# Performance work log

Hardware: AMD Instinct MI355X
Metric: run time of the kernel (lower is better)

## Reference

```python
import jax, jax.numpy as jnp
import numpy as np
import math

SIGMA_DATA = 0.5
SIGMA_MIN = 0.002
SIGMA_MAX = 80.0
B = 32768
STATE = 256
ACT = 64
TD = 16
E = 16
H = 256  # moe hidden = gate_dim = output_dim = hidden_dim//4
IN = STATE + ACT + TD  # 336
TOP_K = 4


def mish(x):
    return x * jnp.tanh(jax.nn.softplus(x))


def setup_inputs() -> dict:
    key = jax.random.key(0)
    ks = jax.random.split(key, 20)
    def xavier(k, shape):
        fan_in, fan_out = shape[-2], shape[-1]
        lim = math.sqrt(6.0 / (fan_in + fan_out))
        return jax.random.uniform(k, shape, jnp.float32, -lim, lim)
    inp = {
        "x": jax.random.normal(ks[0], (B, ACT), jnp.float32),
        "sigma": jax.random.uniform(ks[1], (B,), jnp.float32) * (SIGMA_MAX - SIGMA_MIN) + SIGMA_MIN,
        "state": jax.random.normal(ks[2], (B, STATE), jnp.float32),
        # time MLP: Linear(16,32), Mish, Linear(32,16)
        "tW1": xavier(ks[3], (TD, 2 * TD)), "tb1": jnp.zeros((2 * TD,), jnp.float32),
        "tW2": xavier(ks[4], (2 * TD, TD)), "tb2": jnp.zeros((TD,), jnp.float32),
        # gate: Linear(IN, H), ReLU, (dropout eval), Linear(H, E)
        "gW1": xavier(ks[5], (IN, H)), "gb1": jnp.zeros((H,), jnp.float32),
        "gW2": xavier(ks[6], (H, E)), "gb2": jnp.zeros((E,), jnp.float32),
        # 16 stacked expert MLPs: IN->H->H->H with Mish after each Linear
        "eW1": xavier(ks[7], (E, IN, H)), "eb1": jnp.zeros((E, H), jnp.float32),
        "eW2": xavier(ks[8], (E, H, H)), "eb2": jnp.zeros((E, H), jnp.float32),
        "eW3": xavier(ks[9], (E, H, H)), "eb3": jnp.zeros((E, H), jnp.float32),
        # final layer: Linear(H, ACT)
        "fW": xavier(ks[10], (H, ACT)), "fb": jnp.zeros((ACT,), jnp.float32),
    }
    return inp


def reference(x, sigma, state, tW1, tb1, tW2, tb2, gW1, gb1, gW2, gb2,
              eW1, eb1, eW2, eb2, eW3, eb3, fW, fb):
    # --- consistency-model scalings (boundary condition) ---
    c_skip = SIGMA_DATA ** 2 / ((sigma - SIGMA_MIN) ** 2 + SIGMA_DATA ** 2)
    c_out = (sigma - SIGMA_MIN) * SIGMA_DATA * jax.lax.rsqrt(sigma ** 2 + SIGMA_DATA ** 2)
    c_in = jax.lax.rsqrt(sigma ** 2 + SIGMA_DATA ** 2)
    rescaled_t = 1000.0 * 0.25 * jnp.log(sigma + 1e-44)

    x_in = c_in[:, None] * x

    # --- sinusoidal time embedding (dim=16) + time MLP ---
    half = TD // 2
    freqs = jnp.exp(jnp.arange(half, dtype=jnp.float32) * (-math.log(10000.0) / (half - 1)))
    ang = rescaled_t[:, None] * freqs[None, :]           # [B, 8]
    pe = jnp.concatenate([jnp.sin(ang), jnp.cos(ang)], axis=-1)  # [B, 16]
    t = mish(pe @ tW1 + tb1) @ tW2 + tb2                 # [B, 16]

    inp = jnp.concatenate([x_in, t, state], axis=1)      # [B, 336]

    # --- gate (eval mode: dropout off) ---
    g = jax.nn.relu(inp @ gW1 + gb1) @ gW2 + gb2         # [B, E]
    gate_scores = jax.nn.softmax(g, axis=1)
    top_k_scores, top_k_idx = jax.lax.top_k(gate_scores, TOP_K)  # [B, K]

    # --- run ALL experts densely (as the original does) ---
    h = mish(jnp.einsum('bi,eih->beh', inp, eW1) + eb1)  # [B, E, H]
    h = mish(jnp.einsum('beh,ehk->bek', h, eW2) + eb2)
    expert_out = mish(jnp.einsum('beh,eho->beo', h, eW3) + eb3)  # [B, E, H]

    # --- gather top-k, scale by normalized gate scores, combine ---
    sel = jnp.take_along_axis(expert_out, top_k_idx[:, :, None], axis=1)  # [B, K, H]
    scaled = sel * top_k_scores[:, :, None]
    scaled = scaled / (jnp.sum(top_k_scores, axis=1, keepdims=True)[:, :, None] + 1e-9)
    combined = jnp.sum(scaled, axis=1)                   # [B, H]

    # --- auxiliary loss ---
    one_hot = jax.nn.one_hot(top_k_idx, E, dtype=jnp.float32)  # [B, K, E]
    expert_load = jnp.sum(one_hot, axis=(0, 1)) / (x.shape[0] + 1e-9)
    load_balancing_loss = jnp.var(expert_load, ddof=1)   # torch .var() is unbiased
    entropy = -jnp.mean(jnp.sum(gate_scores * jnp.log(gate_scores + 1e-9), axis=1))
    aux_loss = load_balancing_loss + entropy

    model_out = combined @ fW + fb                       # [B, ACT]
    denoised = c_out[:, None] * model_out + c_skip[:, None] * x
    denoised = jnp.clip(denoised, -1.0, 1.0)             # clip_denoised=True
    return denoised, aux_loss
```

## Files before the change

kernel.cpp:

```cpp
#include <hip/hip_runtime.h>
#include <math.h>

#define BN 32768
#define INDP 352
#define HD 256
#define AD 64
#define EN 16
#define TM 64
#define STOT (BN * 4)

typedef __attribute__((ext_vector_type(8))) short s8v;
typedef __attribute__((ext_vector_type(4))) float f4v;
typedef unsigned short u16;

__device__ __forceinline__ u16 f2bf(float x) {
  unsigned u = __float_as_uint(x);
  return (u16)((u + 0x7fffu + ((u >> 16) & 1u)) >> 16);
}
__device__ __forceinline__ float bf2f(u16 h) { return __uint_as_float(((unsigned)h) << 16); }
__device__ __forceinline__ float rcpf(float a) { float r; asm("v_rcp_f32 %0, %1" : "=v"(r) : "v"(a)); return r; }
__device__ __forceinline__ float mishf(float x) {
  float xc = fminf(x, 30.f);
  float u = __expf(xc);
  float w = fmaf(u, u, u + u);
  return x * w * rcpf(w + 2.f);
}
__device__ __forceinline__ f4v mfma16(s8v a, s8v b, f4v c) {
  return __builtin_amdgcn_mfma_f32_16x16x32_bf16(a, b, c, 0, 0, 0);
}
__device__ __forceinline__ void pack8(const u16* q, u16* d) {
  uint4 u;
  u.x = q[0] | ((unsigned)q[1] << 16); u.y = q[2] | ((unsigned)q[3] << 16);
  u.z = q[4] | ((unsigned)q[5] << 16); u.w = q[6] | ((unsigned)q[7] << 16);
  *(uint4*)d = u;
}

__global__ void k_init(float* __restrict__ out, int* __restrict__ counts,
                       int* __restrict__ cursor, float* __restrict__ ent) {
  int i = blockIdx.x * 256 + threadIdx.x;
  if (i < BN * AD) out[i] = 0.f;
  if (i < 16) { counts[i] = 0; cursor[i] = 0; }
  if (i == 16) *ent = 0.f;
}

__global__ void k_prep(const float* __restrict__ src, u16* __restrict__ dst,
                       int Ksrc, int Spad, int NT, int N,
                       long sStride, long dStride, int NP, int total) {
  int idx = blockIdx.x * 256 + threadIdx.x;
  if (idx >= total) return;
  int l = idx & 63;
  int t = idx >> 6;
  int nt = t % NT; t /= NT;
  int s = t % Spad; t /= Spad;
  int m = t;
  const float* sp = src + (size_t)m * sStride;
  int n = nt * 16 + (l & 15);
  int kb = s * 32 + (l >> 4) * 8;
  u16 q0[8], q1[8], q2[8];
  #pragma unroll
  for (int i = 0; i < 8; ++i) {
    int k = kb + i;
    float v = (k < Ksrc) ? sp[(size_t)k * N + n] : 0.f;
    u16 a = f2bf(v); float r1 = v - bf2f(a);
    u16 b = f2bf(r1); float r2 = r1 - bf2f(b);
    q0[i] = a; q1[i] = b; q2[i] = f2bf(r2);
  }
  u16* d = dst + (size_t)m * dStride + (size_t)((s * NT + nt) * NP) * 512 + l * 8;
  pack8(q0, d);
  pack8(q1, d + 512);
  if (NP == 3) pack8(q2, d + 1024);
}

__global__ void k_time_inp(const float* __restrict__ x, const float* __restrict__ sigma,
                           const float* __restrict__ state,
                           const float* __restrict__ tW1, const float* __restrict__ tb1,
                           const float* __restrict__ tW2, const float* __restrict__ tb2,
                           u16* __restrict__ p0, u16* __restrict__ p1, u16* __restrict__ p2) {
  const int wv = threadIdx.x >> 6;
  const int lane = threadIdx.x & 63;
  const int row = blockIdx.x * 4 + wv;
  const float sg = sigma[row];
  const float rt = 250.0f * logf(sg + 1e-44f);
  float pe = 0.f;
  if (lane < 16) {
    int j = lane & 7;
    float f = expf(-1.3157629102823121f * (float)j);
    float ang = rt * f;
    pe = (lane < 8) ? sinf(ang) : cosf(ang);
  }
  float h1;
  {
    float acc = 0.f;
    int j = lane & 31;
    #pragma unroll
    for (int i = 0; i < 16; ++i) {
      float p = __shfl(pe, i, 64);
      acc = fmaf(p, tW1[i * 32 + j], acc);
    }
    acc += tb1[j];
    float sp = log1pf(expf(acc));
    h1 = acc * tanhf(sp);
  }
  float t2;
  {
    float acc = 0.f;
    int j = lane & 15;
    #pragma unroll
    for (int i = 0; i < 32; ++i) {
      float h = __shfl(h1, i, 64);
      acc = fmaf(h, tW2[i * 16 + j], acc);
    }
    t2 = acc + tb2[j];
  }
  const float c_in = rsqrtf(sg * sg + 0.25f);
  u16* r0 = p0 + (size_t)row * INDP;
  u16* r1 = p1 + (size_t)row * INDP;
  u16* r2 = p2 + (size_t)row * INDP;
  auto wsplit = [&](int c, float v) {
    u16 a = f2bf(v); float ra = v - bf2f(a);
    u16 b = f2bf(ra); float rb = ra - bf2f(b);
    r0[c] = a; r1[c] = b; r2[c] = f2bf(rb);
  };
  wsplit(lane, c_in * x[row * 64 + lane]);
  if (lane < 16) wsplit(64 + lane, t2);
  #pragma unroll
  for (int r = 0; r < 4; ++r)
    wsplit(80 + r * 64 + lane, state[(size_t)row * 256 + r * 64 + lane]);
  if (lane < 16) { r0[336 + lane] = 0; r1[336 + lane] = 0; r2[336 + lane] = 0; }
}

__global__ __launch_bounds__(256) void k_gate(
    const u16* __restrict__ p0, const u16* __restrict__ p1, const u16* __restrict__ p2,
    const u16* __restrict__ gW1b, const float* __restrict__ gb1,
    const float* __restrict__ gW2, const float* __restrict__ gb2,
    int* __restrict__ topk_idx, float* __restrict__ topk_w,
    int* __restrict__ counts, float* __restrict__ ent_sum) {
  __shared__ float sH[TM * 257];
  __shared__ float sB2[256 * 16];
  __shared__ float sLog[TM * 16];
  __shared__ int scnt[16];
  const int tid = threadIdx.x;
  const int l = tid & 63, w = tid >> 6;
  const int g = l >> 4, r16 = l & 15;
  const int row0 = blockIdx.x * TM;
  if (tid < 16) scnt[tid] = 0;

  f4v acc[4][4];
  #pragma unroll
  for (int i = 0; i < 4; ++i)
    #pragma unroll
    for (int j = 0; j < 4; ++j) acc[i][j] = (f4v){0.f, 0.f, 0.f, 0.f};

  for (int s = 0; s < 11; ++s) {
    s8v a0[4], a1[4], a2[4], b0[4], b1[4], b2[4];
    #pragma unroll
    for (int mt = 0; mt < 4; ++mt) {
      size_t off = (size_t)(row0 + mt * 16 + r16) * INDP + s * 32 + g * 8;
      a0[mt] = *(const s8v*)(p0 + off);
      a1[mt] = *(const s8v*)(p1 + off);
      a2[mt] = *(const s8v*)(p2 + off);
    }
    #pragma unroll
    for (int j = 0; j < 4; ++j) {
      const u16* pb = gW1b + (size_t)((s * 16 + w * 4 + j) * 3) * 512 + l * 8;
      b0[j] = *(const s8v*)pb;
      b1[j] = *(const s8v*)(pb + 512);
      b2[j] = *(const s8v*)(pb + 1024);
    }
    #pragma unroll
    for (int mt = 0; mt < 4; ++mt)
      #pragma unroll
      for (int j = 0; j < 4; ++j) {
        acc[mt][j] = mfma16(a0[mt], b0[j], acc[mt][j]);
        acc[mt][j] = mfma16(a0[mt], b1[j], acc[mt][j]);
        acc[mt][j] = mfma16(a1[mt], b0[j], acc[mt][j]);
        acc[mt][j] = mfma16(a1[mt], b1[j], acc[mt][j]);
        acc[mt][j] = mfma16(a0[mt], b2[j], acc[mt][j]);
        acc[mt][j] = mfma16(a2[mt], b0[j], acc[mt][j]);
      }
  }
  float bj[4];
  #pragma unroll
  for (int j = 0; j < 4; ++j) bj[j] = gb1[w * 64 + j * 16 + r16];
  #pragma unroll
  for (int mt = 0; mt < 4; ++mt)
    #pragma unroll
    for (int j = 0; j < 4; ++j)
      #pragma unroll
      for (int r = 0; r < 4; ++r) {
        int row = mt * 16 + g * 4 + r;
        sH[row * 257 + w * 64 + j * 16 + r16] = fmaxf(acc[mt][j][r] + bj[j], 0.f);
      }
  #pragma unroll
  for (int it = 0; it < 4; ++it) {
    int idx = tid + it * 256;
    *(float4*)&sB2[idx * 4] = *(const float4*)(gW2 + (size_t)idx * 4);
  }
  __syncthreads();
  {
    const int rr = tid >> 2, q = tid & 3;
    float g0 = 0.f, g1 = 0.f, g2 = 0.f, g3 = 0.f;
    for (int k = 0; k < 256; ++k) {
      float a = sH[rr * 257 + k];
      float4 bv = *(const float4*)&sB2[k * 16 + q * 4];
      g0 = fmaf(a, bv.x, g0); g1 = fmaf(a, bv.y, g1);
      g2 = fmaf(a, bv.z, g2); g3 = fmaf(a, bv.w, g3);
    }
    sLog[rr * 16 + q * 4 + 0] = g0 + gb2[q * 4 + 0];
    sLog[rr * 16 + q * 4 + 1] = g1 + gb2[q * 4 + 1];
    sLog[rr * 16 + q * 4 + 2] = g2 + gb2[q * 4 + 2];
    sLog[rr * 16 + q * 4 + 3] = g3 + gb2[q * 4 + 3];
  }
  __syncthreads();
  float entc = 0.f;
  if (tid < 64) {
    const int row = row0 + tid;
    float gx[16], mx = -1e30f;
    #pragma unroll
    for (int e = 0; e < 16; ++e) { gx[e] = sLog[tid * 16 + e]; mx = fmaxf(mx, gx[e]); }
    float p[16], s = 0.f;
    #pragma unroll
    for (int e = 0; e < 16; ++e) { p[e] = expf(gx[e] - mx); s += p[e]; }
    const float inv = 1.f / s;
    #pragma unroll
    for (int e = 0; e < 16; ++e) {
      float pr = p[e] * inv;
      entc -= pr * logf(pr + 1e-9f);
    }
    int idxs[4]; float scs[4];
    unsigned used = 0;
    float wsum = 1e-9f;
    #pragma unroll
    for (int k = 0; k < 4; ++k) {
      int be = 0; float bv = -1.f;
      #pragma unroll
      for (int e = 0; e < 16; ++e) {
        float pr = p[e] * inv;
        if (!((used >> e) & 1u) && pr > bv) { bv = pr; be = e; }
      }
      used |= (1u << be);
      idxs[k] = be; scs[k] = bv;
      wsum += bv;
    }
    #pragma unroll
    for (int k = 0; k < 4; ++k) {
      topk_idx[row * 4 + k] = idxs[k];
      topk_w[row * 4 + k] = scs[k] / wsum;
      atomicAdd(&scnt[idxs[k]], 1);
    }
    #pragma unroll
    for (int off = 32; off > 0; off >>= 1) entc += __shfl_down(entc, off, 64);
  }
  __syncthreads();
  if (tid == 0) atomicAdd(ent_sum, entc);
  if (tid < 16 && scnt[tid] > 0) atomicAdd(&counts[tid], scnt[tid]);
}

__global__ void k_aux(const int* __restrict__ counts, const float* __restrict__ ent_sum,
                      int* __restrict__ offsets, int* __restrict__ tbk,
                      float* __restrict__ aux_out) {
  if (threadIdx.x == 0) {
    int off = 0, t = 0;
    float load[16], mean = 0.f;
    for (int e = 0; e < 16; ++e) {
      offsets[e] = off; tbk[e] = t;
      int c = counts[e];
      off += c;
      t += (c + TM - 1) / TM;
      load[e] = (float)c / (32768.0f + 1e-9f);
      mean += load[e];
    }
    offsets[16] = off; tbk[16] = t;
    mean *= (1.f / 16.f);
    float var = 0.f;
    for (int e = 0; e < 16; ++e) { float d = load[e] - mean; var += d * d; }
    var *= (1.f / 15.f);
    *aux_out = var + ent_sum[0] * (1.0f / 32768.0f);
  }
}

__global__ void k_scatter(const int* __restrict__ topk_idx, const float* __restrict__ topk_w,
                          const int* __restrict__ offsets, int* __restrict__ cursor,
                          int* __restrict__ slot_row, float* __restrict__ slot_w) {
  __shared__ int cnt[16];
  __shared__ int base[16];
  const int tid = threadIdx.x;
  if (tid < 16) cnt[tid] = 0;
  __syncthreads();
  const int row = blockIdx.x * 256 + tid;
  int e4[4]; float w4[4]; int lp[4];
  #pragma unroll
  for (int k = 0; k < 4; ++k) {
    e4[k] = topk_idx[row * 4 + k];
    w4[k] = topk_w[row * 4 + k];
    lp[k] = atomicAdd(&cnt[e4[k]], 1);
  }
  __syncthreads();
  if (tid < 16) base[tid] = atomicAdd(&cursor[tid], cnt[tid]);
  __syncthreads();
  #pragma unroll
  for (int k = 0; k < 4; ++k) {
    int s = offsets[e4[k]] + base[e4[k]] + lp[k];
    slot_row[s] = row;
    slot_w[s] = w4[k];
  }
}

__global__ __launch_bounds__(256, 2) void k_expert(
    const u16* __restrict__ inpHi, const u16* __restrict__ inpLo,
    const u16* __restrict__ eW1b, const float* __restrict__ eb1,
    const u16* __restrict__ eW2b, const float* __restrict__ eb2,
    const u16* __restrict__ eW3b, const float* __restrict__ eb3,
    const u16* __restrict__ fWb,
    const int* __restrict__ offsets, const int* __restrict__ counts,
    const int* __restrict__ tbk, const int* __restrict__ slot_row,
    const float* __restrict__ slot_w, float* __restrict__ out) {
  __shared__ __align__(16) u16 sHi[TM * 256];
  __shared__ __align__(16) u16 sLo[TM * 256];
  __shared__ int sRows[TM];
  __shared__ float sWv[TM];

  const int bid = blockIdx.x;
  if (bid >= tbk[16]) return;
  int e = 0;
  #pragma unroll
  for (int i = 1; i < 16; ++i)
    if (bid >= tbk[i]) e = i;
  const int tile = bid - tbk[e];
  const int cnt = counts[e];
  const int s0 = offsets[e] + tile * TM;
  const int nr = min(TM, cnt - tile * TM);
  const int tid = threadIdx.x;
  const int l = tid & 63, w = tid >> 6;
  const int g = l >> 4, r16 = l & 15;
  const int swz = (r16 & 7) << 3;

  if (tid < TM) {
    sRows[tid] = (tid < nr) ? slot_row[s0 + tid] : slot_row[s0];
    sWv[tid] = (tid < nr) ? slot_w[s0 + tid] : 0.f;
  }
  __syncthreads();

  size_t rbase[4];
  #pragma unroll
  for (int mt = 0; mt < 4; ++mt) rbase[mt] = (size_t)sRows[mt * 16 + r16] * INDP;

  f4v acc[4][4];
  #pragma unroll
  for (int i = 0; i < 4; ++i)
    #pragma unroll
    for (int j = 0; j < 4; ++j) acc[i][j] = (f4v){0.f, 0.f, 0.f, 0.f};

  const u16* W1 = eW1b + (size_t)e * 180224;
  for (int s = 0; s < 11; ++s) {
    s8v ah[4], al[4], bh[4], bl[4];
    #pragma unroll
    for (int mt = 0; mt < 4; ++mt) {
      size_t off = rbase[mt] + s * 32 + g * 8;
      ah[mt] = *(const s8v*)(inpHi + off);
      al[mt] = *(const s8v*)(inpLo + off);
    }
    #pragma unroll
    for (int j = 0; j < 4; ++j) {
      const u16* pb = W1 + (size_t)((s * 16 + w * 4 + j) * 2) * 512 + l * 8;
      bh[j] = *(const s8v*)pb;
      bl[j] = *(const s8v*)(pb + 512);
    }
    #pragma unroll
    for (int mt = 0; mt < 4; ++mt)
      #pragma unroll
      for (int j = 0; j < 4; ++j) {
        acc[mt][j] = mfma16(ah[mt], bh[j], acc[mt][j]);
        acc[mt][j] = mfma16(al[mt], bh[j], acc[mt][j]);
        acc[mt][j] = mfma16(ah[mt], bl[j], acc[mt][j]);
      }
  }
  {
    const float* b1 = eb1 + e * HD;
    float bj[4];
    #pragma unroll
    for (int j = 0; j < 4; ++j) bj[j] = b1[w * 64 + j * 16 + r16];
    #pragma unroll
    for (int mt = 0; mt < 4; ++mt)
      #pragma unroll
      for (int j = 0; j < 4; ++j)
        #pragma unroll
        for (int r = 0; r < 4; ++r) {
          int row = mt * 16 + g * 4 + r;
          int col = w * 64 + j * 16 + r16;
          float v = mishf(acc[mt][j][r] + bj[j]);
          u16 h = f2bf(v);
          int ec = col ^ ((row & 7) << 3);
          sHi[row * 256 + ec] = h;
          sLo[row * 256 + ec] = f2bf(v - bf2f(h));
        }
  }
  __syncthreads();

  #pragma unroll 1
  for (int L = 0; L < 2; ++L) {
    const u16* Wb = (L == 0 ? eW2b : eW3b) + (size_t)e * 131072;
    const float* bb = (L == 0 ? eb2 : eb3) + e * HD;
    f4v a2[4][4];
    #pragma unroll
    for (int i = 0; i < 4; ++i)
      #pragma unroll
      for (int j = 0; j < 4; ++j) a2[i][j] = (f4v){0.f, 0.f, 0.f, 0.f};
    #pragma unroll 2
    for (int s = 0; s < 8; ++s) {
      s8v ah[4], al[4], bh[4], bl[4];
      #pragma unroll
      for (int mt = 0; mt < 4; ++mt) {
        int row = mt * 16 + r16;
        int ec = (s * 32 + g * 8) ^ swz;
        ah[mt] = *(const s8v*)&sHi[row * 256 + ec];
        al[mt] = *(const s8v*)&sLo[row * 256 + ec];
      }
      #pragma unroll
      for (int j = 0; j < 4; ++j) {
        const u16* pb = Wb + (size_t)((s * 16 + w * 4 + j) * 2) * 512 + l * 8;
        bh[j] = *(const s8v*)pb;
        bl[j] = *(const s8v*)(pb + 512);
      }
      #pragma unroll
      for (int mt = 0; mt < 4; ++mt)
        #pragma unroll
        for (int j = 0; j < 4; ++j) {
          a2[mt][j] = mfma16(ah[mt], bh[j], a2[mt][j]);
          a2[mt][j] = mfma16(al[mt], bh[j], a2[mt][j]);
          a2[mt][j] = mfma16(ah[mt], bl[j], a2[mt][j]);
        }
    }
    __syncthreads();
    float bj[4];
    #pragma unroll
    for (int j = 0; j < 4; ++j) bj[j] = bb[w * 64 + j * 16 + r16];
    #pragma unroll
    for (int mt = 0; mt < 4; ++mt)
      #pragma unroll
      for (int j = 0; j < 4; ++j)
        #pragma unroll
        for (int r = 0; r < 4; ++r) {
          int row = mt * 16 + g * 4 + r;
          int col = w * 64 + j * 16 + r16;
          float v = mishf(a2[mt][j][r] + bj[j]);
          u16 h = f2bf(v);
          int ec = col ^ ((row & 7) << 3);
          sHi[row * 256 + ec] = h;
          sLo[row * 256 + ec] = f2bf(v - bf2f(h));
        }
    __syncthreads();
  }

  f4v a3[4];
  #pragma unroll
  for (int i = 0; i < 4; ++i) a3[i] = (f4v){0.f, 0.f, 0.f, 0.f};
  #pragma unroll 2
  for (int s = 0; s < 8; ++s) {
    s8v ah[4], al[4];
    #pragma unroll
    for (int mt = 0; mt < 4; ++mt) {
      int row = mt * 16 + r16;
      int ec = (s * 32 + g * 8) ^ swz;
      ah[mt] = *(const s8v*)&sHi[row * 256 + ec];
      al[mt] = *(const s8v*)&sLo[row * 256 + ec];
    }
    const u16* pb = fWb + (size_t)((s * 4 + w) * 2) * 512 + l * 8;
    s8v bh = *(const s8v*)pb;
    s8v bl = *(const s8v*)(pb + 512);
    #pragma unroll
    for (int mt = 0; mt < 4; ++mt) {
      a3[mt] = mfma16(ah[mt], bh, a3[mt]);
      a3[mt] = mfma16(al[mt], bh, a3[mt]);
      a3[mt] = mfma16(ah[mt], bl, a3[mt]);
    }
  }
  #pragma unroll
  for (int mt = 0; mt < 4; ++mt)
    #pragma unroll
    for (int r = 0; r < 4; ++r) {
      int rl = mt * 16 + g * 4 + r;
      if (rl < nr) {
        float v = a3[mt][r] * sWv[rl];
        atomicAdd(&out[(size_t)sRows[rl] * AD + w * 16 + r16], v);
      }
    }
}

__global__ void k_final(const float* __restrict__ x, const float* __restrict__ sigma,
                        const float* __restrict__ fb, float* __restrict__ out) {
  int i = blockIdx.x * 256 + threadIdx.x;
  if (i >= BN * AD) return;
  int row = i >> 6, c = i & 63;
  float sg = sigma[row];
  float sm = sg - 0.002f;
  float c_skip = 0.25f / (sm * sm + 0.25f);
  float c_out = sm * 0.5f * rsqrtf(sg * sg + 0.25f);
  float d = c_out * (out[i] + fb[c]) + c_skip * x[i];
  out[i] = fminf(fmaxf(d, -1.f), 1.f);
}

extern "C" void kernel_launch(void* const* d_in, const int* in_sizes, int n_in,
                              void* d_out, int out_size, void* d_ws, size_t ws_size,
                              hipStream_t stream) {
  const float* x     = (const float*)d_in[0];
  const float* sigma = (const float*)d_in[1];
  const float* state = (const float*)d_in[2];
  const float* tW1   = (const float*)d_in[3];
  const float* tb1   = (const float*)d_in[4];
  const float* tW2   = (const float*)d_in[5];
  const float* tb2   = (const float*)d_in[6];
  const float* gW1   = (const float*)d_in[7];
  const float* gb1   = (const float*)d_in[8];
  const float* gW2   = (const float*)d_in[9];
  const float* gb2   = (const float*)d_in[10];
  const float* eW1   = (const float*)d_in[11];
  const float* eb1   = (const float*)d_in[12];
  const float* eW2   = (const float*)d_in[13];
  const float* eb2   = (const float*)d_in[14];
  const float* eW3   = (const float*)d_in[15];
  const float* eb3   = (const float*)d_in[16];
  const float* fW    = (const float*)d_in[17];
  const float* fb    = (const float*)d_in[18];
  float* out = (float*)d_out;

  char* p = (char*)d_ws;
  auto alloc = [&](size_t bytes) { void* r = (void*)p; p += (bytes + 255) & ~(size_t)255; return r; };
  u16* inpHi  = (u16*)alloc((size_t)BN * INDP * 2);
  u16* inpLo  = (u16*)alloc((size_t)BN * INDP * 2);
  u16* inpMid = (u16*)alloc((size_t)BN * INDP * 2);
  u16* gW1b   = (u16*)alloc((size_t)11 * 16 * 3 * 512 * 2);
  u16* eW1b   = (u16*)alloc((size_t)16 * 180224 * 2);
  u16* eW2b   = (u16*)alloc((size_t)16 * 131072 * 2);
  u16* eW3b   = (u16*)alloc((size_t)16 * 131072 * 2);
  u16* fWb    = (u16*)alloc((size_t)32768 * 2);
  int*   topk_idx = (int*)alloc((size_t)BN * 4 * 4);
  float* topk_w   = (float*)alloc((size_t)BN * 4 * 4);
  int*   counts   = (int*)alloc(64);
  int*   cursor   = (int*)alloc(64);
  int*   offsets  = (int*)alloc(68);
  int*   tbk      = (int*)alloc(68);
  float* ent      = (float*)alloc(4);
  int*   slot_row = (int*)alloc((size_t)STOT * 4);
  float* slot_w   = (float*)alloc((size_t)STOT * 4);

  k_init<<<(BN * AD + 255) / 256, 256, 0, stream>>>(out, counts, cursor, ent);

  int tot;
  tot = 16 * 11 * 16 * 64;
  k_prep<<<(tot + 255) / 256, 256, 0, stream>>>(eW1, eW1b, 336, 11, 16, 256,
                                                (long)336 * 256, 180224, 2, tot);
  tot = 16 * 8 * 16 * 64;
  k_prep<<<(tot + 255) / 256, 256, 0, stream>>>(eW2, eW2b, 256, 8, 16, 256,
                                                (long)256 * 256, 131072, 2, tot);
  k_prep<<<(tot + 255) / 256, 256, 0, stream>>>(eW3, eW3b, 256, 8, 16, 256,
                                                (long)256 * 256, 131072, 2, tot);
  tot = 11 * 16 * 64;
  k_prep<<<(tot + 255) / 256, 256, 0, stream>>>(gW1, gW1b, 336, 11, 16, 256,
                                                0, 0, 3, tot);
  tot = 8 * 4 * 64;
  k_prep<<<(tot + 255) / 256, 256, 0, stream>>>(fW, fWb, 256, 8, 4, 64,
                                                0, 0, 2, tot);

  k_time_inp<<<BN / 4, 256, 0, stream>>>(x, sigma, state, tW1, tb1, tW2, tb2,
                                         inpHi, inpLo, inpMid);
  k_gate<<<BN / TM, 256, 0, stream>>>(inpHi, inpLo, inpMid, gW1b, gb1, gW2, gb2,
                                      topk_idx, topk_w, counts, ent);
  k_aux<<<1, 64, 0, stream>>>(counts, ent, offsets, tbk, out + (size_t)BN * AD);
  k_scatter<<<BN / 256, 256, 0, stream>>>(topk_idx, topk_w, offsets, cursor, slot_row, slot_w);
  k_expert<<<STOT / TM + EN, 256, 0, stream>>>(inpHi, inpLo, eW1b, eb1, eW2b, eb2,
                                               eW3b, eb3, fWb, offsets, counts, tbk,
                                               slot_row, slot_w, out);
  k_final<<<(BN * AD + 255) / 256, 256, 0, stream>>>(x, sigma, fb, out);
}
```

Baseline: 533.1 us.

## Split expert tile across eight waves, pad LDS rows, remap blocks per XCD

The expert kernel moves to 512-thread blocks. The eight waves form a 2x4 grid, so each wave computes two 16-row M tiles instead of four, which halves accumulator registers per wave. LDS rows are padded to 264 elements on top of the existing XOR swizzle. Block IDs are remapped so consecutive tiles of the same expert land on the same XCD chunk, to improve L2 reuse of expert weights. In exchange, each pair of waves now loads the same B fragments separately, and `__launch_bounds__(512,4)` may force a tight VGPR budget and cause spills, while LDS size already caps how many blocks fit per CU.

New measurement: 521.7 us. 2.1% less time.

```diff
diff --git a/kernel.cpp b/kernel.cpp
--- a/kernel.cpp
+++ b/kernel.cpp
@@ -8,6 +8,9 @@
 #define EN 16
 #define TM 64
 #define STOT (BN * 4)
+#define LDP 264
+#define GRID_E 2072
+#define CHUNK_E 259
 
 typedef __attribute__((ext_vector_type(8))) short s8v;
 typedef __attribute__((ext_vector_type(4))) float f4v;
@@ -306,7 +309,7 @@
   }
 }
 
-__global__ __launch_bounds__(256, 2) void k_expert(
+__global__ __launch_bounds__(512, 4) void k_expert(
     const u16* __restrict__ inpHi, const u16* __restrict__ inpLo,
     const u16* __restrict__ eW1b, const float* __restrict__ eb1,
     const u16* __restrict__ eW2b, const float* __restrict__ eb2,
@@ -315,12 +318,12 @@
     const int* __restrict__ offsets, const int* __restrict__ counts,
     const int* __restrict__ tbk, const int* __restrict__ slot_row,
     const float* __restrict__ slot_w, float* __restrict__ out) {
-  __shared__ __align__(16) u16 sHi[TM * 256];
-  __shared__ __align__(16) u16 sLo[TM * 256];
+  __shared__ __align__(16) u16 sHi[TM * LDP];
+  __shared__ __align__(16) u16 sLo[TM * LDP];
   __shared__ int sRows[TM];
   __shared__ float sWv[TM];
 
-  const int bid = blockIdx.x;
+  const int bid = (blockIdx.x & 7) * CHUNK_E + (blockIdx.x >> 3);
   if (bid >= tbk[16]) return;
   int e = 0;
   #pragma unroll
@@ -331,7 +334,10 @@
   const int s0 = offsets[e] + tile * TM;
   const int nr = min(TM, cnt - tile * TM);
   const int tid = threadIdx.x;
-  const int l = tid & 63, w = tid >> 6;
+  const int l = tid & 63;
+  const int w8 = tid >> 6;
+  const int wm = w8 >> 2;
+  const int wn = w8 & 3;
   const int g = l >> 4, r16 = l & 15;
   const int swz = (r16 & 7) << 3;
 
@@ -341,33 +347,34 @@
   }
   __syncthreads();
 
-  size_t rbase[4];
-  #pragma unroll
-  for (int mt = 0; mt < 4; ++mt) rbase[mt] = (size_t)sRows[mt * 16 + r16] * INDP;
-
-  f4v acc[4][4];
-  #pragma unroll
-  for (int i = 0; i < 4; ++i)
+  size_t rbase[2];
+  #pragma unroll
+  for (int mt = 0; mt < 2; ++mt)
+    rbase[mt] = (size_t)sRows[(wm * 2 + mt) * 16 + r16] * INDP;
+
+  f4v acc[2][4];
+  #pragma unroll
+  for (int i = 0; i < 2; ++i)
     #pragma unroll
     for (int j = 0; j < 4; ++j) acc[i][j] = (f4v){0.f, 0.f, 0.f, 0.f};
 
   const u16* W1 = eW1b + (size_t)e * 180224;
   for (int s = 0; s < 11; ++s) {
-    s8v ah[4], al[4], bh[4], bl[4];
-    #pragma unroll
-    for (int mt = 0; mt < 4; ++mt) {
+    s8v ah[2], al[2], bh[4], bl[4];
+    #pragma unroll
+    for (int mt = 0; mt < 2; ++mt) {
       size_t off = rbase[mt] + s * 32 + g * 8;
       ah[mt] = *(const s8v*)(inpHi + off);
       al[mt] = *(const s8v*)(inpLo + off);
     }
     #pragma unroll
     for (int j = 0; j < 4; ++j) {
-      const u16* pb = W1 + (size_t)((s * 16 + w * 4 + j) * 2) * 512 + l * 8;
+      const u16* pb = W1 + (size_t)((s * 16 + wn * 4 + j) * 2) * 512 + l * 8;
       bh[j] = *(const s8v*)pb;
       bl[j] = *(const s8v*)(pb + 512);
     }
     #pragma unroll
-    for (int mt = 0; mt < 4; ++mt)
+    for (int mt = 0; mt < 2; ++mt)
       #pragma unroll
       for (int j = 0; j < 4; ++j) {
         acc[mt][j] = mfma16(ah[mt], bh[j], acc[mt][j]);
@@ -379,20 +386,20 @@
     const float* b1 = eb1 + e * HD;
     float bj[4];
     #pragma unroll
-    for (int j = 0; j < 4; ++j) bj[j] = b1[w * 64 + j * 16 + r16];
-    #pragma unroll
-    for (int mt = 0; mt < 4; ++mt)
+    for (int j = 0; j < 4; ++j) bj[j] = b1[wn * 64 + j * 16 + r16];
+    #pragma unroll
+    for (int mt = 0; mt < 2; ++mt)
       #pragma unroll
       for (int j = 0; j < 4; ++j)
         #pragma unroll
         for (int r = 0; r < 4; ++r) {
-          int row = mt * 16 + g * 4 + r;
-          int col = w * 64 + j * 16 + r16;
+          int row = (wm * 2 + mt) * 16 + g * 4 + r;
+          int col = wn * 64 + j * 16 + r16;
           float v = mishf(acc[mt][j][r] + bj[j]);
           u16 h = f2bf(v);
           int ec = col ^ ((row & 7) << 3);
-          sHi[row * 256 + ec] = h;
-          sLo[row * 256 + ec] = f2bf(v - bf2f(h));
+          sHi[row * LDP + ec] = h;
+          sLo[row * LDP + ec] = f2bf(v - bf2f(h));
         }
   }
   __syncthreads();
@@ -401,29 +408,29 @@
   for (int L = 0; L < 2; ++L) {
     const u16* Wb = (L == 0 ? eW2b : eW3b) + (size_t)e * 131072;
     const float* bb = (L == 0 ? eb2 : eb3) + e * HD;
-    f4v a2[4][4];
-    #pragma unroll
-    for (int i = 0; i < 4; ++i)
+    f4v a2[2][4];
+    #pragma unroll
+    for (int i = 0; i < 2; ++i)
       #pragma unroll
       for (int j = 0; j < 4; ++j) a2[i][j] = (f4v){0.f, 0.f, 0.f, 0.f};
     #pragma unroll 2
     for (int s = 0; s < 8; ++s) {
-      s8v ah[4], al[4], bh[4], bl[4];
-      #pragma unroll
-      for (int mt = 0; mt < 4; ++mt) {
-        int row = mt * 16 + r16;
+      s8v ah[2], al[2], bh[4], bl[4];
+      #pragma unroll
+      for (int mt = 0; mt < 2; ++mt) {
+        int row = (wm * 2 + mt) * 16 + r16;
         int ec = (s * 32 + g * 8) ^ swz;
-        ah[mt] = *(const s8v*)&sHi[row * 256 + ec];
-        al[mt] = *(const s8v*)&sLo[row * 256 + ec];
+        ah[mt] = *(const s8v*)&sHi[row * LDP + ec];
+        al[mt] = *(const s8v*)&sLo[row * LDP + ec];
       }
       #pragma unroll
       for (int j = 0; j < 4; ++j) {
-        const u16* pb = Wb + (size_t)((s * 16 + w * 4 + j) * 2) * 512 + l * 8;
+        const u16* pb = Wb + (size_t)((s * 16 + wn * 4 + j) * 2) * 512 + l * 8;
         bh[j] = *(const s8v*)pb;
         bl[j] = *(const s8v*)(pb + 512);
       }
       #pragma unroll
-      for (int mt = 0; mt < 4; ++mt)
+      for (int mt = 0; mt < 2; ++mt)
         #pragma unroll
         for (int j = 0; j < 4; ++j) {
           a2[mt][j] = mfma16(ah[mt], bh[j], a2[mt][j]);
@@ -434,55 +441,55 @@
     __syncthreads();
     float bj[4];
     #pragma unroll
-    for (int j = 0; j < 4; ++j) bj[j] = bb[w * 64 + j * 16 + r16];
-    #pragma unroll
-    for (int mt = 0; mt < 4; ++mt)
+    for (int j = 0; j < 4; ++j) bj[j] = bb[wn * 64 + j * 16 + r16];
+    #pragma unroll
+    for (int mt = 0; mt < 2; ++mt)
       #pragma unroll
       for (int j = 0; j < 4; ++j)
         #pragma unroll
         for (int r = 0; r < 4; ++r) {
-          int row = mt * 16 + g * 4 + r;
-          int col = w * 64 + j * 16 + r16;
+          int row = (wm * 2 + mt) * 16 + g * 4 + r;
+          int col = wn * 64 + j * 16 + r16;
           float v = mishf(a2[mt][j][r] + bj[j]);
           u16 h = f2bf(v);
           int ec = col ^ ((row & 7) << 3);
-          sHi[row * 256 + ec] = h;
-          sLo[row * 256 + ec] = f2bf(v - bf2f(h));
+          sHi[row * LDP + ec] = h;
+          sLo[row * LDP + ec] = f2bf(v - bf2f(h));
         }
     __syncthreads();
   }
 
-  f4v a3[4];
-  #pragma unroll
-  for (int i = 0; i < 4; ++i) a3[i] = (f4v){0.f, 0.f, 0.f, 0.f};
+  f4v a3[2];
+  #pragma unroll
+  for (int i = 0; i < 2; ++i) a3[i] = (f4v){0.f, 0.f, 0.f, 0.f};
   #pragma unroll 2
   for (int s = 0; s < 8; ++s) {
-    s8v ah[4], al[4];
-    #pragma unroll
-    for (int mt = 0; mt < 4; ++mt) {
-      int row = mt * 16 + r16;
+    s8v ah[2], al[2];
+    #pragma unroll
+    for (int mt = 0; mt < 2; ++mt) {
+      int row = (wm * 2 + mt) * 16 + r16;
       int ec = (s * 32 + g * 8) ^ swz;
-      ah[mt] = *(const s8v*)&sHi[row * 256 + ec];
-      al[mt] = *(const s8v*)&sLo[row * 256 + ec];
-    }
-    const u16* pb = fWb + (size_t)((s * 4 + w) * 2) * 512 + l * 8;
+      ah[mt] = *(const s8v*)&sHi[row * LDP + ec];
+      al[mt] = *(const s8v*)&sLo[row * LDP + ec];
+    }
+    const u16* pb = fWb + (size_t)((s * 4 + wn) * 2) * 512 + l * 8;
     s8v bh = *(const s8v*)pb;
     s8v bl = *(const s8v*)(pb + 512);
     #pragma unroll
-    for (int mt = 0; mt < 4; ++mt) {
+    for (int mt = 0; mt < 2; ++mt) {
       a3[mt] = mfma16(ah[mt], bh, a3[mt]);
       a3[mt] = mfma16(al[mt], bh, a3[mt]);
       a3[mt] = mfma16(ah[mt], bl, a3[mt]);
     }
   }
   #pragma unroll
-  for (int mt = 0; mt < 4; ++mt)
+  for (int mt = 0; mt < 2; ++mt)
     #pragma unroll
     for (int r = 0; r < 4; ++r) {
-      int rl = mt * 16 + g * 4 + r;
+      int rl = (wm * 2 + mt) * 16 + g * 4 + r;
       if (rl < nr) {
         float v = a3[mt][r] * sWv[rl];
-        atomicAdd(&out[(size_t)sRows[rl] * AD + w * 16 + r16], v);
+        atomicAdd(&out[(size_t)sRows[rl] * AD + wn * 16 + r16], v);
       }
     }
 }
@@ -568,8 +575,8 @@
                                       topk_idx, topk_w, counts, ent);
   k_aux<<<1, 64, 0, stream>>>(counts, ent, offsets, tbk, out + (size_t)BN * AD);
   k_scatter<<<BN / 256, 256, 0, stream>>>(topk_idx, topk_w, offsets, cursor, slot_row, slot_w);
-  k_expert<<<STOT / TM + EN, 256, 0, stream>>>(inpHi, inpLo, eW1b, eb1, eW2b, eb2,
-                                               eW3b, eb3, fWb, offsets, counts, tbk,
-                                               slot_row, slot_w, out);
+  k_expert<<<GRID_E, 512, 0, stream>>>(inpHi, inpLo, eW1b, eb1, eW2b, eb2,
+                                       eW3b, eb3, fWb, offsets, counts, tbk,
+                                       slot_row, slot_w, out);
   k_final<<<(BN * AD + 255) / 256, 256, 0, stream>>>(x, sigma, fb, out);
 }
```
